# Performance work log

Measured on AMD Instinct MI355X. Metric: run time of the kernel, lower is better.

## Reference

```python
import jax, jax.numpy as jnp
import numpy as np

N = 2048          # nodes
IN_DIM = 512      # in_dim
H = 8             # num_heads
HD = IN_DIM // H  # head_dim = 64
L = 5             # max_path_len
E = 32768         # edges
D_EDGE = 64       # edge_feat_dim


def setup_inputs() -> dict:
    key = jax.random.key(0)
    ks = jax.random.split(key, 14)
    w = 1.0 / np.sqrt(IN_DIM)
    return {
        "node_feat": jax.random.normal(ks[0], (N, IN_DIM), jnp.float32),
        "edge_index": jax.random.randint(ks[1], (2, E), 0, N, dtype=jnp.int32),
        "max_path_len": 5,
        "shortest_distances": jax.random.randint(ks[2], (N, N), 0, L + 1, dtype=jnp.int32),
        "shortest_paths": jax.random.randint(ks[3], (N, N, L), 0, E + 1, dtype=jnp.int32),  # E == padding row
        "edge_feat": jax.random.normal(ks[4], (E, D_EDGE), jnp.float32),
        "attention_mask": jnp.zeros((N, N), jnp.int32),
        "WQ": jax.random.normal(ks[5], (IN_DIM, IN_DIM), jnp.float32) * w,
        "bQ": jax.random.normal(ks[6], (IN_DIM,), jnp.float32) * 0.02,
        "WK": jax.random.normal(ks[7], (IN_DIM, IN_DIM), jnp.float32) * w,
        "bK": jax.random.normal(ks[8], (IN_DIM,), jnp.float32) * 0.02,
        "WV": jax.random.normal(ks[9], (IN_DIM, IN_DIM), jnp.float32) * w,
        "bV": jax.random.normal(ks[10], (IN_DIM,), jnp.float32) * 0.02,
        "WO": jax.random.normal(ks[11], (IN_DIM, IN_DIM), jnp.float32) * w,
        "bO": jnp.zeros((IN_DIM,), jnp.float32),
        "spatial_bias": jax.random.normal(ks[12], ((L + 1) * H, 1), jnp.float32) * 0.02,
        "edge_weight": jax.random.normal(ks[13], ((L + 1) * H, D_EDGE), jnp.float32) * 0.02,
    }


def reference(node_feat, edge_index, max_path_len, shortest_distances, shortest_paths,
              edge_feat, attention_mask, WQ, bQ, WK, bK, WV, bV, WO, bO,
              spatial_bias, edge_weight):
    Nn, D = node_feat.shape
    Lp = max_path_len  # min(max_path_len, max_shortest_path_len); distances reach Lp here

    Q = (node_feat @ WQ + bQ).reshape(Nn, H, HD)
    K = (node_feat @ WK + bK).reshape(Nn, H, HD)
    V = (node_feat @ WV + bV).reshape(Nn, H, HD)

    # QK^T / sqrt(head_dim), laid out [N, N, H] as in the original after permute
    scores = jnp.einsum('nhd,mhd->nmh', Q, K) / np.sqrt(HD).astype(np.float32)

    # SpatialEncoding: bias table [(L+1)*H, 1] -> [L+1, H]; gather by clamped distance
    sp_table = spatial_bias.reshape(Lp + 1, H)
    dist = jnp.clip(shortest_distances, 0, Lp)
    scores = scores + sp_table[dist]  # [N, N, H]

    # EdgeEncoding: einsum('xyld,ldh->xyh') refactored as per-edge projection then gather
    W_e = edge_weight[: Lp * H].reshape(Lp, H, D_EDGE)  # (reshape[L,H,D].permute -> [L,D,H])
    padded = jnp.concatenate([edge_feat, jnp.zeros((1, D_EDGE), edge_feat.dtype)], axis=0)
    T = jnp.einsum('ed,lhd->elh', padded, W_e)  # [E+1, L, H]
    sp = shortest_paths[:, :, :Lp]
    gathered = T[sp, jnp.arange(Lp)[None, None, :]]  # [N, N, L, H]
    scores = scores + gathered.sum(axis=2)

    mask = attention_mask.astype(bool)
    scores = jnp.where(mask[:, :, None], -jnp.inf, scores)

    # NOTE: original applies softmax over dim=-1 of the [N, N, H] tensor (the head axis);
    # faithfully reproduced here. Dropout is identity (eval / p for inference).
    attn = jax.nn.softmax(scores, axis=-1)

    out = jnp.einsum('nmh,mhd->nhd', attn, V).reshape(Nn, D)
    return out @ WO + bO
```

## Files before the change

### kernel.cpp

```cpp
#include <hip/hip_runtime.h>

#define NN     2048
#define DIM    512
#define NH     8
#define HD     64
#define NE     32768
#define EPAD   32832
#define CHUNKS 4
#define LOG2E  1.4426950408889634f

typedef __attribute__((ext_vector_type(8))) short bf16x8;
typedef __attribute__((ext_vector_type(4))) float f32x4;

#define MFMA(a,b,c) __builtin_amdgcn_mfma_f32_16x16x32_bf16((a),(b),(c),0,0,0)

__device__ __forceinline__ float bf2f(unsigned int u16){
  union { unsigned int i; float f; } v; v.i = u16 << 16; return v.f;
}
__device__ __forceinline__ unsigned short f2bf(float f){
  union { float ff; unsigned int i; } v; v.ff = f;
  return (unsigned short)((v.i + 0x7fffu + ((v.i >> 16) & 1u)) >> 16);
}

__global__ __launch_bounds__(256) void cvt_k(
    const float* __restrict__ X, const float* __restrict__ ef, const float* __restrict__ ew,
    unsigned short* __restrict__ Xb, unsigned short* __restrict__ pEF, unsigned short* __restrict__ pEW)
{
  long g = (long)blockIdx.x*256 + threadIdx.x;
  const long GX = (long)NN*DIM/8;
  const long GE = (long)EPAD*8;
  const float* src; unsigned short* dst; long off, lim8;
  if (g < GX){ src = X;  dst = Xb;  off = g;        lim8 = GX; }
  else if (g < GX+GE){ src = ef; dst = pEF; off = g-GX; lim8 = (long)NE*8; }
  else { off = g-GX-GE; if (off >= 512) return; src = ew; dst = pEW; lim8 = 320; }
  unsigned short o[8];
  if (off < lim8){
    #pragma unroll
    for (int i=0;i<8;i++) o[i] = f2bf(src[off*8+i]);
  } else {
    #pragma unroll
    for (int i=0;i<8;i++) o[i] = 0;
  }
  *(uint4*)(dst + off*8) = *(const uint4*)o;
}

__global__ __launch_bounds__(256) void transpose512(
    const float* __restrict__ a0, const float* __restrict__ a1,
    const float* __restrict__ a2, const float* __restrict__ a3,
    unsigned short* __restrict__ out)
{
  __shared__ unsigned short tile[32][33];
  const float* src = blockIdx.z==0 ? a0 : blockIdx.z==1 ? a1 : blockIdx.z==2 ? a2 : a3;
  unsigned short* dst = out + (size_t)blockIdx.z*DIM*DIM;
  int bx = blockIdx.x*32, by = blockIdx.y*32;
  int tx = threadIdx.x, ty = threadIdx.y;
  #pragma unroll
  for (int i=0;i<32;i+=8) tile[ty+i][tx] = f2bf(src[(size_t)(by+ty+i)*DIM + bx+tx]);
  __syncthreads();
  #pragma unroll
  for (int i=0;i<32;i+=8) dst[(size_t)(bx+ty+i)*DIM + by+tx] = tile[tx][ty+i];
}

__global__ __launch_bounds__(256) void gemm_bt(
    const unsigned short* __restrict__ A1, const unsigned short* __restrict__ A2,
    const float* __restrict__ bias, unsigned short* __restrict__ C, float* __restrict__ Cf,
    int M, int N, int K, int bias_row)
{
  int lane = threadIdx.x & 63, w = threadIdx.x >> 6;
  int quad = lane >> 4, low = lane & 15;
  int m0 = blockIdx.y*64 + w*16;
  int n0 = blockIdx.x*64;
  f32x4 acc[4];
  #pragma unroll
  for (int t=0;t<4;t++) acc[t] = (f32x4){0.f,0.f,0.f,0.f};
  for (int k0=0; k0<K; k0+=32){
    bf16x8 a = *(const bf16x8*)(A1 + (size_t)(m0+low)*K + k0 + quad*8);
    #pragma unroll
    for (int t=0;t<4;t++){
      bf16x8 b = *(const bf16x8*)(A2 + (size_t)(n0+16*t+low)*K + k0 + quad*8);
      acc[t] = MFMA(a, b, acc[t]);
    }
  }
  #pragma unroll
  for (int t=0;t<4;t++){
    #pragma unroll
    for (int r=0;r<4;r++){
      int row = m0 + quad*4 + r;
      int col = n0 + 16*t + low;
      float v = acc[t][r];
      if (bias) v += bias[bias_row ? row : col];
      if (Cf) Cf[(size_t)row*N + col] = v;
      else    C [(size_t)row*N + col] = f2bf(v);
    }
  }
}

__global__ __launch_bounds__(512) void attn_k(
    const unsigned short* __restrict__ Qb, const unsigned short* __restrict__ Kb,
    const unsigned short* __restrict__ Vt, const unsigned short* __restrict__ T2,
    const float* __restrict__ spb, const int* __restrict__ dist,
    const int* __restrict__ sp, const int* __restrict__ maskp,
    float* __restrict__ partO)
{
  __shared__ __attribute__((aligned(16))) float sld[NH][16][68];
  __shared__ float sptab[48];
  int tid = threadIdx.x;
  int lane = tid & 63, h = tid >> 6;
  int quad = lane >> 4, low = lane & 15;
  int q0 = blockIdx.x * 16;
  int chunk = blockIdx.y;
  if (tid < 48) sptab[tid] = spb[tid];

  bf16x8 aq[2];
  #pragma unroll
  for (int s=0;s<2;s++)
    aq[s] = *(const bf16x8*)(Qb + (size_t)(q0+low)*DIM + h*HD + s*32 + quad*8);

  f32x4 accO[4];
  #pragma unroll
  for (int t=0;t<4;t++) accO[t] = (f32x4){0.f,0.f,0.f,0.f};

  for (int jt=0; jt<8; ++jt){
    int m0 = chunk*512 + jt*64;
    __syncthreads();

    #pragma unroll
    for (int it=0; it<2; ++it){
      int p = tid + it*512;
      int qq = p >> 6, mm = p & 63;
      long pix = (long)(q0+qq)*NN + (m0+mm);
      int dd = dist[pix];
      dd = dd < 0 ? 0 : (dd > 5 ? 5 : dd);
      float b[8];
      #pragma unroll
      for (int x=0;x<8;x++) b[x] = sptab[dd*8 + x];
      #pragma unroll
      for (int l=0;l<5;l++){
        int e = sp[pix*5 + l];
        if ((unsigned)e > (unsigned)NE) e = NE;
        uint4 tv = *(const uint4*)(T2 + (size_t)e*64 + l*8);
        b[0] += bf2f(tv.x & 0xffffu); b[1] += bf2f(tv.x >> 16);
        b[2] += bf2f(tv.y & 0xffffu); b[3] += bf2f(tv.y >> 16);
        b[4] += bf2f(tv.z & 0xffffu); b[5] += bf2f(tv.z >> 16);
        b[6] += bf2f(tv.w & 0xffffu); b[7] += bf2f(tv.w >> 16);
      }
      int msk = maskp[pix];
      #pragma unroll
      for (int x=0;x<8;x++) sld[x][qq][mm] = msk ? -1e30f : b[x];
    }
    __syncthreads();

    f32x4 S[4];
    #pragma unroll
    for (int t=0;t<4;t++) S[t] = (f32x4){0.f,0.f,0.f,0.f};
    #pragma unroll
    for (int s=0;s<2;s++){
      #pragma unroll
      for (int t=0;t<4;t++){
        bf16x8 bk = *(const bf16x8*)(Kb + (size_t)(m0+16*t+low)*DIM + h*HD + s*32 + quad*8);
        S[t] = MFMA(aq[s], bk, S[t]);
      }
    }
    #pragma unroll
    for (int t=0;t<4;t++){
      #pragma unroll
      for (int r=0;r<4;r++){
        float* slot = &sld[h][quad*4+r][low+16*t];
        *slot = S[t][r]*0.125f + *slot;
      }
    }
    __syncthreads();

    #pragma unroll
    for (int it=0; it<2; ++it){
      int p = tid + it*512;
      int qq = p >> 6, mm = p & 63;
      float s0[8];
      #pragma unroll
      for (int x=0;x<8;x++) s0[x] = sld[x][qq][mm];
      float mx = s0[0];
      #pragma unroll
      for (int x=1;x<8;x++) mx = fmaxf(mx, s0[x]);
      float sum = 0.f;
      #pragma unroll
      for (int x=0;x<8;x++){ s0[x] = exp2f((s0[x]-mx)*LOG2E); sum += s0[x]; }
      float inv = (mx < -1e29f) ? 0.f : 1.f/sum;
      #pragma unroll
      for (int x=0;x<8;x++) sld[x][qq][mm] = s0[x]*inv;
    }
    __syncthreads();

    bf16x8 ap[2];
    #pragma unroll
    for (int s=0;s<2;s++){
      const float* pp = &sld[h][low][s*32 + quad*8];
      float4 x0 = *(const float4*)pp;
      float4 x1 = *(const float4*)(pp + 4);
      bf16x8 a;
      a[0]=(short)f2bf(x0.x); a[1]=(short)f2bf(x0.y); a[2]=(short)f2bf(x0.z); a[3]=(short)f2bf(x0.w);
      a[4]=(short)f2bf(x1.x); a[5]=(short)f2bf(x1.y); a[6]=(short)f2bf(x1.z); a[7]=(short)f2bf(x1.w);
      ap[s] = a;
    }
    #pragma unroll
    for (int s=0;s<2;s++){
      #pragma unroll
      for (int t=0;t<4;t++){
        bf16x8 bv = *(const bf16x8*)(Vt + (size_t)(h*HD + 16*t + low)*NN + m0 + s*32 + quad*8);
        accO[t] = MFMA(ap[s], bv, accO[t]);
      }
    }
  }

  #pragma unroll
  for (int t=0;t<4;t++){
    #pragma unroll
    for (int r=0;r<4;r++){
      int q = quad*4 + r;
      partO[(((size_t)chunk*NN + q0 + q)*NH + h)*HD + 16*t + low] = accO[t][r];
    }
  }
}

__global__ __launch_bounds__(512) void merge_k(const float* __restrict__ partO,
                                               unsigned short* __restrict__ Obf)
{
  size_t idx = (size_t)blockIdx.x*512 + threadIdx.x;
  float s = 0.f;
  #pragma unroll
  for (int c=0;c<CHUNKS;c++) s += partO[(size_t)c*NN*DIM + idx];
  Obf[idx] = f2bf(s);
}

extern "C" void kernel_launch(void* const* d_in, const int* in_sizes, int n_in,
                              void* d_out, int out_size, void* d_ws, size_t ws_size,
                              hipStream_t stream)
{
  const float* X    = (const float*)d_in[0];
  const int*  dist  = (const int*)d_in[3];
  const int*  sp    = (const int*)d_in[4];
  const float* ef   = (const float*)d_in[5];
  const int*  maskp = (const int*)d_in[6];
  const float* WQ   = (const float*)d_in[7];
  const float* bQ   = (const float*)d_in[8];
  const float* WK   = (const float*)d_in[9];
  const float* bK   = (const float*)d_in[10];
  const float* WV   = (const float*)d_in[11];
  const float* bV   = (const float*)d_in[12];
  const float* WO   = (const float*)d_in[13];
  const float* bO   = (const float*)d_in[14];
  const float* spb  = (const float*)d_in[15];
  const float* ew   = (const float*)d_in[16];

  char* ws = (char*)d_ws;
  unsigned short* Wt   = (unsigned short*)(ws + 0);
  unsigned short* Xb   = (unsigned short*)(ws + 2097152);
  unsigned short* Qb   = (unsigned short*)(ws + 4194304);
  unsigned short* Kb   = (unsigned short*)(ws + 6291456);
  unsigned short* Vtb  = (unsigned short*)(ws + 8388608);
  unsigned short* pEF  = (unsigned short*)(ws + 10485760);
  unsigned short* pEW  = (unsigned short*)(ws + 14688256);
  unsigned short* T2   = (unsigned short*)(ws + 14696448);
  unsigned short* Obf  = (unsigned short*)(ws + 18898944);
  float*          pO   = (float*)(ws + 20996096);

  cvt_k<<<dim3(1540), dim3(256), 0, stream>>>(X, ef, ew, Xb, pEF, pEW);
  transpose512<<<dim3(16,16,4), dim3(32,8), 0, stream>>>(WQ, WK, WV, WO, Wt);
  gemm_bt<<<dim3(1,513),  dim3(256), 0, stream>>>(pEF, pEW, (const float*)nullptr, T2, (float*)nullptr, EPAD, 64, 64, 0);
  gemm_bt<<<dim3(8,32),   dim3(256), 0, stream>>>(Xb,  Wt,          bQ, Qb,  (float*)nullptr, NN, DIM, DIM, 0);
  gemm_bt<<<dim3(8,32),   dim3(256), 0, stream>>>(Xb,  Wt + 262144, bK, Kb,  (float*)nullptr, NN, DIM, DIM, 0);
  gemm_bt<<<dim3(32,8),   dim3(256), 0, stream>>>(Wt + 524288, Xb,  bV, Vtb, (float*)nullptr, DIM, NN, DIM, 1);
  attn_k<<<dim3(128,CHUNKS), dim3(512), 0, stream>>>(Qb, Kb, Vtb, T2, spb, dist, sp, maskp, pO);
  merge_k<<<dim3(2048), dim3(512), 0, stream>>>(pO, Obf);
  gemm_bt<<<dim3(8,32),  dim3(256), 0, stream>>>(Obf, Wt + 786432, bO, (unsigned short*)nullptr, (float*)d_out, NN, DIM, DIM, 0);
}
```

Before: 434.0 us.

## Precompute edge/spatial bias in separate kernel and split attention into more chunks

Moves the gather of the spatial and edge-path bias out of the attention kernel into a dedicated bias_k pass. That pass reads a per-path-position T2L layout and writes a bf16 [N,N,8] bias buffer. The new attention kernel uses 8 chunks, prefetches the next bias tile in registers, and writes bf16 partials. The Q and K projections are merged into one GEMM. The change aims to remove the irregular gather latency from the MFMA loop and raise parallelism, at the cost of a 64MB bias buffer round trip and extra bf16 rounding, and it falls back to the old path when the workspace is too small.

```diff
diff --git a/kernel.cpp b/kernel.cpp
--- a/kernel.cpp
+++ b/kernel.cpp
@@ -2,11 +2,13 @@
 
 #define NN     2048
 #define DIM    512
+#define QKS    1024
 #define NH     8
 #define HD     64
 #define NE     32768
 #define EPAD   32832
 #define CHUNKS 4
+#define CH2    8
 #define LOG2E  1.4426950408889634f
 
 typedef __attribute__((ext_vector_type(8))) short bf16x8;
@@ -63,7 +65,8 @@
 
 __global__ __launch_bounds__(256) void gemm_bt(
     const unsigned short* __restrict__ A1, const unsigned short* __restrict__ A2,
-    const float* __restrict__ bias, unsigned short* __restrict__ C, float* __restrict__ Cf,
+    const float* __restrict__ biasA, const float* __restrict__ biasB,
+    unsigned short* __restrict__ C, float* __restrict__ Cf,
     int M, int N, int K, int bias_row)
 {
   int lane = threadIdx.x & 63, w = threadIdx.x >> 6;
@@ -88,9 +91,182 @@
       int row = m0 + quad*4 + r;
       int col = n0 + 16*t + low;
       float v = acc[t][r];
-      if (bias) v += bias[bias_row ? row : col];
+      if (biasA){
+        int bi = bias_row ? row : col;
+        v += (bi < 512) ? biasA[bi] : biasB[bi-512];
+      }
       if (Cf) Cf[(size_t)row*N + col] = v;
       else    C [(size_t)row*N + col] = f2bf(v);
+    }
+  }
+}
+
+__global__ __launch_bounds__(256) void t2_k(
+    const unsigned short* __restrict__ pEF, const unsigned short* __restrict__ pEW,
+    unsigned short* __restrict__ T2, unsigned short* __restrict__ T2L)
+{
+  int lane = threadIdx.x & 63, w = threadIdx.x >> 6;
+  int quad = lane >> 4, low = lane & 15;
+  int m0 = blockIdx.y*64 + w*16;
+  f32x4 acc[4];
+  #pragma unroll
+  for (int t=0;t<4;t++) acc[t] = (f32x4){0.f,0.f,0.f,0.f};
+  #pragma unroll
+  for (int k0=0; k0<64; k0+=32){
+    bf16x8 a = *(const bf16x8*)(pEF + (size_t)(m0+low)*64 + k0 + quad*8);
+    #pragma unroll
+    for (int t=0;t<4;t++){
+      bf16x8 b = *(const bf16x8*)(pEW + (size_t)(16*t+low)*64 + k0 + quad*8);
+      acc[t] = MFMA(a, b, acc[t]);
+    }
+  }
+  #pragma unroll
+  for (int t=0;t<4;t++){
+    #pragma unroll
+    for (int r=0;r<4;r++){
+      int row = m0 + quad*4 + r;
+      int col = 16*t + low;
+      unsigned short v = f2bf(acc[t][r]);
+      T2[(size_t)row*64 + col] = v;
+      if (col < 40)
+        T2L[((size_t)(col>>3)*EPAD + row)*8 + (col&7)] = v;
+    }
+  }
+}
+
+__global__ __launch_bounds__(256) void bias_k(
+    const float* __restrict__ spb, const int* __restrict__ dist,
+    const int* __restrict__ sp, const int* __restrict__ maskp,
+    const unsigned short* __restrict__ T2L, unsigned short* __restrict__ biasBuf)
+{
+  int pix = blockIdx.x*256 + threadIdx.x;
+  int dd = dist[pix];
+  dd = dd < 0 ? 0 : (dd > 5 ? 5 : dd);
+  int msk = maskp[pix];
+  float b[8];
+  #pragma unroll
+  for (int x=0;x<8;x++) b[x] = spb[dd*8 + x];
+  #pragma unroll
+  for (int l=0;l<5;l++){
+    int e = sp[(size_t)pix*5 + l];
+    if ((unsigned)e > (unsigned)NE) e = NE;
+    uint4 tv = *(const uint4*)(T2L + ((size_t)l*EPAD + e)*8);
+    b[0] += bf2f(tv.x & 0xffffu); b[1] += bf2f(tv.x >> 16);
+    b[2] += bf2f(tv.y & 0xffffu); b[3] += bf2f(tv.y >> 16);
+    b[4] += bf2f(tv.z & 0xffffu); b[5] += bf2f(tv.z >> 16);
+    b[6] += bf2f(tv.w & 0xffffu); b[7] += bf2f(tv.w >> 16);
+  }
+  unsigned short o[8];
+  #pragma unroll
+  for (int x=0;x<8;x++) o[x] = f2bf(msk ? -1e30f : b[x]);
+  *(uint4*)(biasBuf + (size_t)pix*8) = *(const uint4*)o;
+}
+
+__global__ __launch_bounds__(512, 8) void attn2_k(
+    const unsigned short* __restrict__ Qb, const unsigned short* __restrict__ Kb,
+    const unsigned short* __restrict__ Vt, const unsigned short* __restrict__ biasBuf,
+    unsigned short* __restrict__ partO)
+{
+  __shared__ __attribute__((aligned(16))) float sld[NH][16][68];
+  int tid = threadIdx.x;
+  int lane = tid & 63, h = tid >> 6;
+  int quad = lane >> 4, low = lane & 15;
+  int q0 = blockIdx.x * 16;
+  int chunk = blockIdx.y;
+
+  bf16x8 aq[2];
+  #pragma unroll
+  for (int s=0;s<2;s++)
+    aq[s] = *(const bf16x8*)(Qb + (size_t)(q0+low)*QKS + h*HD + s*32 + quad*8);
+
+  f32x4 accO[4];
+  #pragma unroll
+  for (int t=0;t<4;t++) accO[t] = (f32x4){0.f,0.f,0.f,0.f};
+
+  uint4 bpf[2];
+  #pragma unroll
+  for (int it=0; it<2; ++it){
+    int p = tid + it*512; int qq = p >> 6, mm = p & 63;
+    bpf[it] = *(const uint4*)(biasBuf + ((size_t)(q0+qq)*NN + chunk*256 + mm)*8);
+  }
+
+  for (int jt=0; jt<4; ++jt){
+    int m0 = chunk*256 + jt*64;
+    __syncthreads();
+
+    f32x4 S[4];
+    #pragma unroll
+    for (int t=0;t<4;t++) S[t] = (f32x4){0.f,0.f,0.f,0.f};
+    #pragma unroll
+    for (int s=0;s<2;s++){
+      #pragma unroll
+      for (int t=0;t<4;t++){
+        bf16x8 bk = *(const bf16x8*)(Kb + (size_t)(m0+16*t+low)*QKS + h*HD + s*32 + quad*8);
+        S[t] = MFMA(aq[s], bk, S[t]);
+      }
+    }
+    #pragma unroll
+    for (int t=0;t<4;t++){
+      #pragma unroll
+      for (int r=0;r<4;r++)
+        sld[h][quad*4+r][low+16*t] = S[t][r]*0.125f;
+    }
+    __syncthreads();
+
+    #pragma unroll
+    for (int it=0; it<2; ++it){
+      int p = tid + it*512;
+      int qq = p >> 6, mm = p & 63;
+      uint4 bv = bpf[it];
+      if (jt < 3)
+        bpf[it] = *(const uint4*)(biasBuf + ((size_t)(q0+qq)*NN + m0 + 64 + mm)*8);
+      float bb[8];
+      bb[0]=bf2f(bv.x & 0xffffu); bb[1]=bf2f(bv.x >> 16);
+      bb[2]=bf2f(bv.y & 0xffffu); bb[3]=bf2f(bv.y >> 16);
+      bb[4]=bf2f(bv.z & 0xffffu); bb[5]=bf2f(bv.z >> 16);
+      bb[6]=bf2f(bv.w & 0xffffu); bb[7]=bf2f(bv.w >> 16);
+      float s0[8];
+      #pragma unroll
+      for (int x=0;x<8;x++) s0[x] = sld[x][qq][mm] + bb[x];
+      float mx = s0[0];
+      #pragma unroll
+      for (int x=1;x<8;x++) mx = fmaxf(mx, s0[x]);
+      float sum = 0.f;
+      #pragma unroll
+      for (int x=0;x<8;x++){ s0[x] = exp2f((s0[x]-mx)*LOG2E); sum += s0[x]; }
+      float inv = (mx < -1e29f) ? 0.f : 1.f/sum;
+      #pragma unroll
+      for (int x=0;x<8;x++) sld[x][qq][mm] = s0[x]*inv;
+    }
+    __syncthreads();
+
+    bf16x8 ap[2];
+    #pragma unroll
+    for (int s=0;s<2;s++){
+      const float* pp = &sld[h][low][s*32 + quad*8];
+      float4 x0 = *(const float4*)pp;
+      float4 x1 = *(const float4*)(pp + 4);
+      bf16x8 a;
+      a[0]=(short)f2bf(x0.x); a[1]=(short)f2bf(x0.y); a[2]=(short)f2bf(x0.z); a[3]=(short)f2bf(x0.w);
+      a[4]=(short)f2bf(x1.x); a[5]=(short)f2bf(x1.y); a[6]=(short)f2bf(x1.z); a[7]=(short)f2bf(x1.w);
+      ap[s] = a;
+    }
+    #pragma unroll
+    for (int s=0;s<2;s++){
+      #pragma unroll
+      for (int t=0;t<4;t++){
+        bf16x8 bv = *(const bf16x8*)(Vt + (size_t)(h*HD + 16*t + low)*NN + m0 + s*32 + quad*8);
+        accO[t] = MFMA(ap[s], bv, accO[t]);
+      }
+    }
+  }
+
+  #pragma unroll
+  for (int t=0;t<4;t++){
+    #pragma unroll
+    for (int r=0;r<4;r++){
+      int q = quad*4 + r;
+      partO[((size_t)chunk*NN + q0 + q)*DIM + h*HD + 16*t + low] = f2bf(accO[t][r]);
     }
   }
 }
@@ -114,7 +290,7 @@
   bf16x8 aq[2];
   #pragma unroll
   for (int s=0;s<2;s++)
-    aq[s] = *(const bf16x8*)(Qb + (size_t)(q0+low)*DIM + h*HD + s*32 + quad*8);
+    aq[s] = *(const bf16x8*)(Qb + (size_t)(q0+low)*QKS + h*HD + s*32 + quad*8);
 
   f32x4 accO[4];
   #pragma unroll
@@ -157,7 +333,7 @@
     for (int s=0;s<2;s++){
       #pragma unroll
       for (int t=0;t<4;t++){
-        bf16x8 bk = *(const bf16x8*)(Kb + (size_t)(m0+16*t+low)*DIM + h*HD + s*32 + quad*8);
+        bf16x8 bk = *(const bf16x8*)(Kb + (size_t)(m0+16*t+low)*QKS + h*HD + s*32 + quad*8);
         S[t] = MFMA(aq[s], bk, S[t]);
       }
     }
@@ -216,18 +392,19 @@
     #pragma unroll
     for (int r=0;r<4;r++){
       int q = quad*4 + r;
-      partO[(((size_t)chunk*NN + q0 + q)*NH + h)*HD + 16*t + low] = accO[t][r];
-    }
-  }
-}
-
-__global__ __launch_bounds__(512) void merge_k(const float* __restrict__ partO,
-                                               unsigned short* __restrict__ Obf)
+      partO[((size_t)chunk*NN + q0 + q)*DIM + h*HD + 16*t + low] = accO[t][r];
+    }
+  }
+}
+
+__global__ __launch_bounds__(512) void merge_k(const unsigned short* __restrict__ pb,
+                                               const float* __restrict__ pf,
+                                               int chunks, unsigned short* __restrict__ Obf)
 {
   size_t idx = (size_t)blockIdx.x*512 + threadIdx.x;
   float s = 0.f;
-  #pragma unroll
-  for (int c=0;c<CHUNKS;c++) s += partO[(size_t)c*NN*DIM + idx];
+  if (pb){ for (int c=0;c<chunks;c++) s += bf2f(pb[(size_t)c*NN*DIM + idx]); }
+  else   { for (int c=0;c<chunks;c++) s += pf[(size_t)c*NN*DIM + idx]; }
   Obf[idx] = f2bf(s);
 }
 
@@ -254,22 +431,34 @@
   char* ws = (char*)d_ws;
   unsigned short* Wt   = (unsigned short*)(ws + 0);
   unsigned short* Xb   = (unsigned short*)(ws + 2097152);
-  unsigned short* Qb   = (unsigned short*)(ws + 4194304);
-  unsigned short* Kb   = (unsigned short*)(ws + 6291456);
+  unsigned short* QKb  = (unsigned short*)(ws + 4194304);
   unsigned short* Vtb  = (unsigned short*)(ws + 8388608);
   unsigned short* pEF  = (unsigned short*)(ws + 10485760);
   unsigned short* pEW  = (unsigned short*)(ws + 14688256);
   unsigned short* T2   = (unsigned short*)(ws + 14696448);
-  unsigned short* Obf  = (unsigned short*)(ws + 18898944);
-  float*          pO   = (float*)(ws + 20996096);
+  unsigned short* T2L  = (unsigned short*)(ws + 18898944);
+  unsigned short* Obf  = (unsigned short*)(ws + 21525504);
+  char*           pMem = ws + 23622656;
+  unsigned short* biasBuf = (unsigned short*)(ws + 40399872);
+  const size_t NEED_BIG = 40399872ULL + 67108864ULL;
 
   cvt_k<<<dim3(1540), dim3(256), 0, stream>>>(X, ef, ew, Xb, pEF, pEW);
   transpose512<<<dim3(16,16,4), dim3(32,8), 0, stream>>>(WQ, WK, WV, WO, Wt);
-  gemm_bt<<<dim3(1,513),  dim3(256), 0, stream>>>(pEF, pEW, (const float*)nullptr, T2, (float*)nullptr, EPAD, 64, 64, 0);
-  gemm_bt<<<dim3(8,32),   dim3(256), 0, stream>>>(Xb,  Wt,          bQ, Qb,  (float*)nullptr, NN, DIM, DIM, 0);
-  gemm_bt<<<dim3(8,32),   dim3(256), 0, stream>>>(Xb,  Wt + 262144, bK, Kb,  (float*)nullptr, NN, DIM, DIM, 0);
-  gemm_bt<<<dim3(32,8),   dim3(256), 0, stream>>>(Wt + 524288, Xb,  bV, Vtb, (float*)nullptr, DIM, NN, DIM, 1);
-  attn_k<<<dim3(128,CHUNKS), dim3(512), 0, stream>>>(Qb, Kb, Vtb, T2, spb, dist, sp, maskp, pO);
-  merge_k<<<dim3(2048), dim3(512), 0, stream>>>(pO, Obf);
-  gemm_bt<<<dim3(8,32),  dim3(256), 0, stream>>>(Obf, Wt + 786432, bO, (unsigned short*)nullptr, (float*)d_out, NN, DIM, DIM, 0);
-}
+  t2_k<<<dim3(1,513), dim3(256), 0, stream>>>(pEF, pEW, T2, T2L);
+  gemm_bt<<<dim3(16,32), dim3(256), 0, stream>>>(Xb, Wt, bQ, bK, QKb, (float*)nullptr, NN, QKS, DIM, 0);
+  gemm_bt<<<dim3(32,8), dim3(256), 0, stream>>>(Wt + 524288, Xb, bV, (const float*)nullptr, Vtb, (float*)nullptr, DIM, NN, DIM, 1);
+
+  if (ws_size >= NEED_BIG){
+    unsigned short* pObf = (unsigned short*)pMem;
+    bias_k<<<dim3(16384), dim3(256), 0, stream>>>(spb, dist, sp, maskp, T2L, biasBuf);
+    attn2_k<<<dim3(128,CH2), dim3(512), 0, stream>>>(QKb, QKb + 512, Vtb, biasBuf, pObf);
+    merge_k<<<dim3(2048), dim3(512), 0, stream>>>(pObf, (const float*)nullptr, CH2, Obf);
+  } else {
+    float* pO = (float*)pMem;
+    attn_k<<<dim3(128,CHUNKS), dim3(512), 0, stream>>>(QKb, QKb + 512, Vtb, T2, spb, dist, sp, maskp, pO);
+    merge_k<<<dim3(2048), dim3(512), 0, stream>>>((const unsigned short*)nullptr, pO, CHUNKS, Obf);
+  }
+
+  gemm_bt<<<dim3(8,32), dim3(256), 0, stream>>>(Obf, Wt + 786432, bO, (const float*)nullptr,
+                                                (unsigned short*)nullptr, (float*)d_out, NN, DIM, DIM, 0);
+}
```

Measured after the change: 495.0 us. 14.1% more time.

## Split bias gather into separate kernel and fuse Q/K projections

Applied to the files above, without the earlier changes.

Moves the spatial and edge bias gather out of the attention kernel into a dedicated bias_k pass. That pass writes a bf16 bias buffer of 8 heads per pixel, and the edge projection table T2 is relaid out per path position so each lookup reads 16 bytes. The Q and K projections become one GEMM with concatenated weights and a dual bias. The attention kernel now prefetches bias tiles, keeps scores and probabilities in bf16 shared memory, uses 8 key chunks instead of 4, and writes bf16 partial outputs. The intent is to decouple the latency-bound random gather from the MFMA loop and raise occupancy. The cost is an extra round trip through a 64MB bias buffer and lower precision in the partial sums.

```diff
diff --git a/kernel.cpp b/kernel.cpp
--- a/kernel.cpp
+++ b/kernel.cpp
@@ -2,11 +2,12 @@
 
 #define NN     2048
 #define DIM    512
+#define QKS    1024
 #define NH     8
 #define HD     64
 #define NE     32768
 #define EPAD   32832
-#define CHUNKS 4
+#define CH2    8
 #define LOG2E  1.4426950408889634f
 
 typedef __attribute__((ext_vector_type(8))) short bf16x8;
@@ -63,7 +64,8 @@
 
 __global__ __launch_bounds__(256) void gemm_bt(
     const unsigned short* __restrict__ A1, const unsigned short* __restrict__ A2,
-    const float* __restrict__ bias, unsigned short* __restrict__ C, float* __restrict__ Cf,
+    const float* __restrict__ biasA, const float* __restrict__ biasB,
+    unsigned short* __restrict__ C, float* __restrict__ Cf,
     int M, int N, int K, int bias_row)
 {
   int lane = threadIdx.x & 63, w = threadIdx.x >> 6;
@@ -88,96 +90,152 @@
       int row = m0 + quad*4 + r;
       int col = n0 + 16*t + low;
       float v = acc[t][r];
-      if (bias) v += bias[bias_row ? row : col];
+      if (biasA){
+        int bi = bias_row ? row : col;
+        v += (bi < 512) ? biasA[bi] : biasB[bi-512];
+      }
       if (Cf) Cf[(size_t)row*N + col] = v;
       else    C [(size_t)row*N + col] = f2bf(v);
     }
   }
 }
 
-__global__ __launch_bounds__(512) void attn_k(
-    const unsigned short* __restrict__ Qb, const unsigned short* __restrict__ Kb,
-    const unsigned short* __restrict__ Vt, const unsigned short* __restrict__ T2,
+__global__ __launch_bounds__(256) void t2_k(
+    const unsigned short* __restrict__ pEF, const unsigned short* __restrict__ pEW,
+    unsigned short* __restrict__ T2L)
+{
+  int lane = threadIdx.x & 63, w = threadIdx.x >> 6;
+  int quad = lane >> 4, low = lane & 15;
+  int m0 = blockIdx.y*64 + w*16;
+  f32x4 acc[4];
+  #pragma unroll
+  for (int t=0;t<4;t++) acc[t] = (f32x4){0.f,0.f,0.f,0.f};
+  #pragma unroll
+  for (int k0=0; k0<64; k0+=32){
+    bf16x8 a = *(const bf16x8*)(pEF + (size_t)(m0+low)*64 + k0 + quad*8);
+    #pragma unroll
+    for (int t=0;t<4;t++){
+      bf16x8 b = *(const bf16x8*)(pEW + (size_t)(16*t+low)*64 + k0 + quad*8);
+      acc[t] = MFMA(a, b, acc[t]);
+    }
+  }
+  #pragma unroll
+  for (int t=0;t<4;t++){
+    #pragma unroll
+    for (int r=0;r<4;r++){
+      int row = m0 + quad*4 + r;
+      int col = 16*t + low;
+      if (col < 40)
+        T2L[((size_t)(col>>3)*EPAD + row)*8 + (col&7)] = f2bf(acc[t][r]);
+    }
+  }
+}
+
+__global__ __launch_bounds__(256) void bias_k(
     const float* __restrict__ spb, const int* __restrict__ dist,
     const int* __restrict__ sp, const int* __restrict__ maskp,
-    float* __restrict__ partO)
-{
-  __shared__ __attribute__((aligned(16))) float sld[NH][16][68];
-  __shared__ float sptab[48];
+    const unsigned short* __restrict__ T2L, unsigned short* __restrict__ biasBuf)
+{
+  int pix = blockIdx.x*256 + threadIdx.x;
+  int dd = dist[pix];
+  int msk = maskp[pix];
+  const int* spp = sp + (size_t)pix*5;
+  int e0 = spp[0], e1 = spp[1], e2 = spp[2], e3 = spp[3], e4 = spp[4];
+  if ((unsigned)e0 > (unsigned)NE) e0 = NE;
+  if ((unsigned)e1 > (unsigned)NE) e1 = NE;
+  if ((unsigned)e2 > (unsigned)NE) e2 = NE;
+  if ((unsigned)e3 > (unsigned)NE) e3 = NE;
+  if ((unsigned)e4 > (unsigned)NE) e4 = NE;
+  uint4 t0 = *(const uint4*)(T2L + ((size_t)0*EPAD + e0)*8);
+  uint4 t1 = *(const uint4*)(T2L + ((size_t)1*EPAD + e1)*8);
+  uint4 t2 = *(const uint4*)(T2L + ((size_t)2*EPAD + e2)*8);
+  uint4 t3 = *(const uint4*)(T2L + ((size_t)3*EPAD + e3)*8);
+  uint4 t4 = *(const uint4*)(T2L + ((size_t)4*EPAD + e4)*8);
+  dd = dd < 0 ? 0 : (dd > 5 ? 5 : dd);
+  float b[8];
+  #pragma unroll
+  for (int x=0;x<8;x++) b[x] = spb[dd*8 + x];
+  b[0] += bf2f(t0.x & 0xffffu) + bf2f(t1.x & 0xffffu) + bf2f(t2.x & 0xffffu) + bf2f(t3.x & 0xffffu) + bf2f(t4.x & 0xffffu);
+  b[1] += bf2f(t0.x >> 16)     + bf2f(t1.x >> 16)     + bf2f(t2.x >> 16)     + bf2f(t3.x >> 16)     + bf2f(t4.x >> 16);
+  b[2] += bf2f(t0.y & 0xffffu) + bf2f(t1.y & 0xffffu) + bf2f(t2.y & 0xffffu) + bf2f(t3.y & 0xffffu) + bf2f(t4.y & 0xffffu);
+  b[3] += bf2f(t0.y >> 16)     + bf2f(t1.y >> 16)     + bf2f(t2.y >> 16)     + bf2f(t3.y >> 16)     + bf2f(t4.y >> 16);
+  b[4] += bf2f(t0.z & 0xffffu) + bf2f(t1.z & 0xffffu) + bf2f(t2.z & 0xffffu) + bf2f(t3.z & 0xffffu) + bf2f(t4.z & 0xffffu);
+  b[5] += bf2f(t0.z >> 16)     + bf2f(t1.z >> 16)     + bf2f(t2.z >> 16)     + bf2f(t3.z >> 16)     + bf2f(t4.z >> 16);
+  b[6] += bf2f(t0.w & 0xffffu) + bf2f(t1.w & 0xffffu) + bf2f(t2.w & 0xffffu) + bf2f(t3.w & 0xffffu) + bf2f(t4.w & 0xffffu);
+  b[7] += bf2f(t0.w >> 16)     + bf2f(t1.w >> 16)     + bf2f(t2.w >> 16)     + bf2f(t3.w >> 16)     + bf2f(t4.w >> 16);
+  unsigned short o[8];
+  #pragma unroll
+  for (int x=0;x<8;x++) o[x] = f2bf(msk ? -1e30f : b[x]);
+  *(uint4*)(biasBuf + (size_t)pix*8) = *(const uint4*)o;
+}
+
+__global__ __launch_bounds__(512) void attn2_k(
+    const unsigned short* __restrict__ Qb, const unsigned short* __restrict__ Kb,
+    const unsigned short* __restrict__ Vt, const unsigned short* __restrict__ biasBuf,
+    unsigned short* __restrict__ partO)
+{
+  __shared__ __attribute__((aligned(16))) unsigned short sldb[NH][16][72];
   int tid = threadIdx.x;
   int lane = tid & 63, h = tid >> 6;
   int quad = lane >> 4, low = lane & 15;
   int q0 = blockIdx.x * 16;
   int chunk = blockIdx.y;
-  if (tid < 48) sptab[tid] = spb[tid];
 
   bf16x8 aq[2];
   #pragma unroll
   for (int s=0;s<2;s++)
-    aq[s] = *(const bf16x8*)(Qb + (size_t)(q0+low)*DIM + h*HD + s*32 + quad*8);
+    aq[s] = *(const bf16x8*)(Qb + (size_t)(q0+low)*QKS + h*HD + s*32 + quad*8);
 
   f32x4 accO[4];
   #pragma unroll
   for (int t=0;t<4;t++) accO[t] = (f32x4){0.f,0.f,0.f,0.f};
 
-  for (int jt=0; jt<8; ++jt){
-    int m0 = chunk*512 + jt*64;
+  uint4 bpf[2];
+  #pragma unroll
+  for (int it=0; it<2; ++it){
+    int p = tid + it*512; int qq = p >> 6, mm = p & 63;
+    bpf[it] = *(const uint4*)(biasBuf + ((size_t)(q0+qq)*NN + chunk*256 + mm)*8);
+  }
+
+  for (int jt=0; jt<4; ++jt){
+    int m0 = chunk*256 + jt*64;
+    __syncthreads();
+
+    f32x4 S[4];
+    #pragma unroll
+    for (int t=0;t<4;t++) S[t] = (f32x4){0.f,0.f,0.f,0.f};
+    #pragma unroll
+    for (int s=0;s<2;s++){
+      #pragma unroll
+      for (int t=0;t<4;t++){
+        bf16x8 bk = *(const bf16x8*)(Kb + (size_t)(m0+16*t+low)*QKS + h*HD + s*32 + quad*8);
+        S[t] = MFMA(aq[s], bk, S[t]);
+      }
+    }
+    #pragma unroll
+    for (int t=0;t<4;t++){
+      #pragma unroll
+      for (int r=0;r<4;r++)
+        sldb[h][quad*4+r][low+16*t] = f2bf(S[t][r]*0.125f);
+    }
     __syncthreads();
 
     #pragma unroll
     for (int it=0; it<2; ++it){
       int p = tid + it*512;
       int qq = p >> 6, mm = p & 63;
-      long pix = (long)(q0+qq)*NN + (m0+mm);
-      int dd = dist[pix];
-      dd = dd < 0 ? 0 : (dd > 5 ? 5 : dd);
-      float b[8];
-      #pragma unroll
-      for (int x=0;x<8;x++) b[x] = sptab[dd*8 + x];
-      #pragma unroll
-      for (int l=0;l<5;l++){
-        int e = sp[pix*5 + l];
-        if ((unsigned)e > (unsigned)NE) e = NE;
-        uint4 tv = *(const uint4*)(T2 + (size_t)e*64 + l*8);
-        b[0] += bf2f(tv.x & 0xffffu); b[1] += bf2f(tv.x >> 16);
-        b[2] += bf2f(tv.y & 0xffffu); b[3] += bf2f(tv.y >> 16);
-        b[4] += bf2f(tv.z & 0xffffu); b[5] += bf2f(tv.z >> 16);
-        b[6] += bf2f(tv.w & 0xffffu); b[7] += bf2f(tv.w >> 16);
-      }
-      int msk = maskp[pix];
-      #pragma unroll
-      for (int x=0;x<8;x++) sld[x][qq][mm] = msk ? -1e30f : b[x];
-    }
-    __syncthreads();
-
-    f32x4 S[4];
-    #pragma unroll
-    for (int t=0;t<4;t++) S[t] = (f32x4){0.f,0.f,0.f,0.f};
-    #pragma unroll
-    for (int s=0;s<2;s++){
-      #pragma unroll
-      for (int t=0;t<4;t++){
-        bf16x8 bk = *(const bf16x8*)(Kb + (size_t)(m0+16*t+low)*DIM + h*HD + s*32 + quad*8);
-        S[t] = MFMA(aq[s], bk, S[t]);
-      }
-    }
-    #pragma unroll
-    for (int t=0;t<4;t++){
-      #pragma unroll
-      for (int r=0;r<4;r++){
-        float* slot = &sld[h][quad*4+r][low+16*t];
-        *slot = S[t][r]*0.125f + *slot;
-      }
-    }
-    __syncthreads();
-
-    #pragma unroll
-    for (int it=0; it<2; ++it){
-      int p = tid + it*512;
-      int qq = p >> 6, mm = p & 63;
+      uint4 bv = bpf[it];
+      if (jt < 3)
+        bpf[it] = *(const uint4*)(biasBuf + ((size_t)(q0+qq)*NN + m0 + 64 + mm)*8);
       float s0[8];
-      #pragma unroll
-      for (int x=0;x<8;x++) s0[x] = sld[x][qq][mm];
+      s0[0] = bf2f(sldb[0][qq][mm]) + bf2f(bv.x & 0xffffu);
+      s0[1] = bf2f(sldb[1][qq][mm]) + bf2f(bv.x >> 16);
+      s0[2] = bf2f(sldb[2][qq][mm]) + bf2f(bv.y & 0xffffu);
+      s0[3] = bf2f(sldb[3][qq][mm]) + bf2f(bv.y >> 16);
+      s0[4] = bf2f(sldb[4][qq][mm]) + bf2f(bv.z & 0xffffu);
+      s0[5] = bf2f(sldb[5][qq][mm]) + bf2f(bv.z >> 16);
+      s0[6] = bf2f(sldb[6][qq][mm]) + bf2f(bv.w & 0xffffu);
+      s0[7] = bf2f(sldb[7][qq][mm]) + bf2f(bv.w >> 16);
       float mx = s0[0];
       #pragma unroll
       for (int x=1;x<8;x++) mx = fmaxf(mx, s0[x]);
@@ -186,27 +244,17 @@
       for (int x=0;x<8;x++){ s0[x] = exp2f((s0[x]-mx)*LOG2E); sum += s0[x]; }
       float inv = (mx < -1e29f) ? 0.f : 1.f/sum;
       #pragma unroll
-      for (int x=0;x<8;x++) sld[x][qq][mm] = s0[x]*inv;
+      for (int x=0;x<8;x++) sldb[x][qq][mm] = f2bf(s0[x]*inv);
     }
     __syncthreads();
 
-    bf16x8 ap[2];
     #pragma unroll
     for (int s=0;s<2;s++){
-      const float* pp = &sld[h][low][s*32 + quad*8];
-      float4 x0 = *(const float4*)pp;
-      float4 x1 = *(const float4*)(pp + 4);
-      bf16x8 a;
-      a[0]=(short)f2bf(x0.x); a[1]=(short)f2bf(x0.y); a[2]=(short)f2bf(x0.z); a[3]=(short)f2bf(x0.w);
-      a[4]=(short)f2bf(x1.x); a[5]=(short)f2bf(x1.y); a[6]=(short)f2bf(x1.z); a[7]=(short)f2bf(x1.w);
-      ap[s] = a;
-    }
-    #pragma unroll
-    for (int s=0;s<2;s++){
+      bf16x8 ap = *(const bf16x8*)&sldb[h][low][s*32 + quad*8];
       #pragma unroll
       for (int t=0;t<4;t++){
         bf16x8 bv = *(const bf16x8*)(Vt + (size_t)(h*HD + 16*t + low)*NN + m0 + s*32 + quad*8);
-        accO[t] = MFMA(ap[s], bv, accO[t]);
+        accO[t] = MFMA(ap, bv, accO[t]);
       }
     }
   }
@@ -216,18 +264,18 @@
     #pragma unroll
     for (int r=0;r<4;r++){
       int q = quad*4 + r;
-      partO[(((size_t)chunk*NN + q0 + q)*NH + h)*HD + 16*t + low] = accO[t][r];
-    }
-  }
-}
-
-__global__ __launch_bounds__(512) void merge_k(const float* __restrict__ partO,
+      partO[((size_t)chunk*NN + q0 + q)*DIM + h*HD + 16*t + low] = f2bf(accO[t][r]);
+    }
+  }
+}
+
+__global__ __launch_bounds__(512) void merge_k(const unsigned short* __restrict__ pb,
                                                unsigned short* __restrict__ Obf)
 {
   size_t idx = (size_t)blockIdx.x*512 + threadIdx.x;
   float s = 0.f;
   #pragma unroll
-  for (int c=0;c<CHUNKS;c++) s += partO[(size_t)c*NN*DIM + idx];
+  for (int c=0;c<CH2;c++) s += bf2f(pb[(size_t)c*NN*DIM + idx]);
   Obf[idx] = f2bf(s);
 }
 
@@ -252,24 +300,25 @@
   const float* ew   = (const float*)d_in[16];
 
   char* ws = (char*)d_ws;
-  unsigned short* Wt   = (unsigned short*)(ws + 0);
-  unsigned short* Xb   = (unsigned short*)(ws + 2097152);
-  unsigned short* Qb   = (unsigned short*)(ws + 4194304);
-  unsigned short* Kb   = (unsigned short*)(ws + 6291456);
-  unsigned short* Vtb  = (unsigned short*)(ws + 8388608);
-  unsigned short* pEF  = (unsigned short*)(ws + 10485760);
-  unsigned short* pEW  = (unsigned short*)(ws + 14688256);
-  unsigned short* T2   = (unsigned short*)(ws + 14696448);
-  unsigned short* Obf  = (unsigned short*)(ws + 18898944);
-  float*          pO   = (float*)(ws + 20996096);
+  unsigned short* Wt      = (unsigned short*)(ws + 0);
+  unsigned short* Xb      = (unsigned short*)(ws + 2097152);
+  unsigned short* QKb     = (unsigned short*)(ws + 4194304);
+  unsigned short* Vtb     = (unsigned short*)(ws + 8388608);
+  unsigned short* pEF     = (unsigned short*)(ws + 10485760);
+  unsigned short* pEW     = (unsigned short*)(ws + 14688256);
+  unsigned short* T2L     = (unsigned short*)(ws + 14696448);
+  unsigned short* Obf     = (unsigned short*)(ws + 17323008);
+  unsigned short* partO   = (unsigned short*)(ws + 19420160);
+  unsigned short* biasBuf = (unsigned short*)(ws + 36197376);
 
   cvt_k<<<dim3(1540), dim3(256), 0, stream>>>(X, ef, ew, Xb, pEF, pEW);
   transpose512<<<dim3(16,16,4), dim3(32,8), 0, stream>>>(WQ, WK, WV, WO, Wt);
-  gemm_bt<<<dim3(1,513),  dim3(256), 0, stream>>>(pEF, pEW, (const float*)nullptr, T2, (float*)nullptr, EPAD, 64, 64, 0);
-  gemm_bt<<<dim3(8,32),   dim3(256), 0, stream>>>(Xb,  Wt,          bQ, Qb,  (float*)nullptr, NN, DIM, DIM, 0);
-  gemm_bt<<<dim3(8,32),   dim3(256), 0, stream>>>(Xb,  Wt + 262144, bK, Kb,  (float*)nullptr, NN, DIM, DIM, 0);
-  gemm_bt<<<dim3(32,8),   dim3(256), 0, stream>>>(Wt + 524288, Xb,  bV, Vtb, (float*)nullptr, DIM, NN, DIM, 1);
-  attn_k<<<dim3(128,CHUNKS), dim3(512), 0, stream>>>(Qb, Kb, Vtb, T2, spb, dist, sp, maskp, pO);
-  merge_k<<<dim3(2048), dim3(512), 0, stream>>>(pO, Obf);
-  gemm_bt<<<dim3(8,32),  dim3(256), 0, stream>>>(Obf, Wt + 786432, bO, (unsigned short*)nullptr, (float*)d_out, NN, DIM, DIM, 0);
-}
+  t2_k<<<dim3(1,513), dim3(256), 0, stream>>>(pEF, pEW, T2L);
+  gemm_bt<<<dim3(16,32), dim3(256), 0, stream>>>(Xb, Wt, bQ, bK, QKb, (float*)nullptr, NN, QKS, DIM, 0);
+  gemm_bt<<<dim3(32,8), dim3(256), 0, stream>>>(Wt + 524288, Xb, bV, (const float*)nullptr, Vtb, (float*)nullptr, DIM, NN, DIM, 1);
+  bias_k<<<dim3(16384), dim3(256), 0, stream>>>(spb, dist, sp, maskp, T2L, biasBuf);
+  attn2_k<<<dim3(128,CH2), dim3(512), 0, stream>>>(QKb, QKb + 512, Vtb, biasBuf, partO);
+  merge_k<<<dim3(2048), dim3(512), 0, stream>>>(partO, Obf);
+  gemm_bt<<<dim3(8,32), dim3(256), 0, stream>>>(Obf, Wt + 786432, bO, (const float*)nullptr,
+                                                (unsigned short*)nullptr, (float*)d_out, NN, DIM, DIM, 0);
+}
```

Result: no change. 439.5 us (+1.3%).
